# Performance work log

Hardware: AMD Instinct MI355X
Metric: run time of the kernel (lower is better)

Reference implementation:

```python
import jax, jax.numpy as jnp
import numpy as np

DIM = 1024
NUM_HEADS = 16
HEAD_DIM = DIM // NUM_HEADS
SCALE = HEAD_DIM ** (-0.5)


def setup_inputs() -> dict:
    key = jax.random.key(0)
    ks = jax.random.split(key, 10)
    b, nq, nkv = 1, 4096, 4096
    s = DIM ** -0.5
    return {
        "q": jax.random.normal(ks[0], (b, nq, DIM), jnp.float32),
        "kv": jax.random.normal(ks[1], (b, nkv, DIM), jnp.float32),
        "q_w": jax.random.normal(ks[2], (DIM, DIM), jnp.float32) * s,
        "q_b": jnp.zeros((DIM,), jnp.float32),
        "k_w": jax.random.normal(ks[3], (DIM, DIM), jnp.float32) * s,
        "k_b": jnp.zeros((DIM,), jnp.float32),
        "v_w": jax.random.normal(ks[4], (DIM, DIM), jnp.float32) * s,
        "v_b": jnp.zeros((DIM,), jnp.float32),
        "o_w": jax.random.normal(ks[5], (DIM, DIM), jnp.float32) * s,
        "o_b": jnp.zeros((DIM,), jnp.float32),
    }


def reference(q, kv, q_w, q_b, k_w, k_b, v_w, v_b, o_w, o_b):
    b, nq, _ = q.shape
    nkv = kv.shape[1]
    h, c = NUM_HEADS, HEAD_DIM
    # projections (torch Linear: x @ W^T + b); split into heads
    qh = (q @ q_w.T + q_b).reshape(b, nq, h, c).transpose(0, 2, 1, 3)   # b h nq c
    kh = (kv @ k_w.T + k_b).reshape(b, nkv, h, c).transpose(0, 2, 1, 3)  # b h nkv c
    vh = (kv @ v_w.T + v_b).reshape(b, nkv, h, c).transpose(0, 2, 1, 3)  # b h nkv c
    # full attention score matrix (non-fused, as in source)
    attn = jnp.einsum('bhqc,bhkc->bhqk', qh, kh) * SCALE
    attn = jax.nn.softmax(attn, axis=-1)
    out = jnp.einsum('bhqk,bhkc->bhqc', attn, vh)  # b h nq c
    out = out.transpose(0, 2, 1, 3).reshape(b, nq, h * c)
    out = out @ o_w.T + o_b
    return out
```

## Files before the change

### kernel.cpp

```cpp
#include <hip/hip_runtime.h>


typedef unsigned short ushort_t;
typedef unsigned short ushort4v __attribute__((ext_vector_type(4)));
typedef unsigned short ushort8 __attribute__((ext_vector_type(8)));
typedef __bf16 bf16x8 __attribute__((ext_vector_type(8)));
typedef float f32x4 __attribute__((ext_vector_type(4)));
typedef float f32x16 __attribute__((ext_vector_type(16)));
typedef unsigned int uint4v __attribute__((ext_vector_type(4)));

#define SEQ 4096
#define DIM 1024
#define NH 16
#define HD 64
#define QSCALE 0.18033688011112042f

#define LSTR 40
#define ABUF (128 * LSTR)
#define BBUF (64 * LSTR)

__device__ inline ushort_t fcvt(float f) {
    return __builtin_bit_cast(ushort_t, (__bf16)f);
}
__device__ inline bf16x8 frag_of(ushort8 t) {
    return __builtin_bit_cast(bf16x8, t);
}
__device__ inline bf16x8 lds_frag(const ushort_t* p) {
    return frag_of(*(const ushort8*)p);
}
__device__ inline unsigned pk2(float a, float b) {
    return (unsigned)fcvt(a) | ((unsigned)fcvt(b) << 16);
}
__device__ inline void plswap(unsigned& a, unsigned& b) {
    asm("v_permlane32_swap_b32 %0, %1" : "+v"(a), "+v"(b));
}
__device__ inline int swz(int row, int col) {
    return row * 64 + (col ^ ((row & 7) << 3));
}

__global__ __launch_bounds__(256) void cvt2(
    const float* __restrict__ s0, ushort_t* __restrict__ d0,
    const float* __restrict__ s1, ushort_t* __restrict__ d1, int n8)
{
    const float* s = blockIdx.y ? s1 : s0;
    ushort_t*    d = blockIdx.y ? d1 : d0;
    int i = blockIdx.x * 256 + threadIdx.x;
    if (i >= n8) return;
    const f32x4* sp = (const f32x4*)s + (size_t)i * 2;
    f32x4 a = sp[0], b = sp[1];
    ushort8 o;
    for (int k = 0; k < 4; ++k) { o[k] = fcvt(a[k]); o[k + 4] = fcvt(b[k]); }
    *((ushort8*)d + i) = o;
}

__global__ __launch_bounds__(256) void cvt4(
    const float* __restrict__ s0, ushort_t* __restrict__ d0,
    const float* __restrict__ s1, ushort_t* __restrict__ d1,
    const float* __restrict__ s2, ushort_t* __restrict__ d2,
    const float* __restrict__ s3, ushort_t* __restrict__ d3, int n8)
{
    const float* ss[4] = {s0, s1, s2, s3};
    ushort_t*    dd[4] = {d0, d1, d2, d3};
    const float* s = ss[blockIdx.y];
    ushort_t*    d = dd[blockIdx.y];
    int i = blockIdx.x * 256 + threadIdx.x;
    if (i >= n8) return;
    const f32x4* sp = (const f32x4*)s + (size_t)i * 2;
    f32x4 a = sp[0], b = sp[1];
    ushort8 o;
    for (int k = 0; k < 4; ++k) { o[k] = fcvt(a[k]); o[k + 4] = fcvt(b[k]); }
    *((ushort8*)d + i) = o;
}

__device__ __attribute__((always_inline)) inline void gemm_core(
    const ushort_t* __restrict__ A, const ushort_t* __restrict__ W,
    int m0, int n0, int tid, f32x4 (&acc)[4][2], ushort_t* sA, ushort_t* sB)
{
    const int lane = tid & 63;
    const int quad = lane >> 4;
    const int l15  = lane & 15;
    const int wm   = (tid >> 6) >> 1;
    const int wn   = (tid >> 6) & 1;

    const int ar0 = tid >> 2;
    const int ar1 = (tid + 256) >> 2;
    const int ac  = (tid & 3) << 3;
    const int br  = tid >> 2;
    const ushort_t* Ag0 = A + (size_t)(m0 + ar0) * DIM + ac;
    const ushort_t* Ag1 = A + (size_t)(m0 + ar1) * DIM + ac;
    const ushort_t* Wg  = W + (size_t)(n0 + br) * DIM + ac;
    const int la0 = ar0 * LSTR + ac, la1 = ar1 * LSTR + ac, lb = br * LSTR + ac;

    *(ushort8*)(sA + la0) = *(const ushort8*)(Ag0);
    *(ushort8*)(sA + la1) = *(const ushort8*)(Ag1);
    *(ushort8*)(sB + lb)  = *(const ushort8*)(Wg);
    __syncthreads();

    for (int it = 0; it < DIM / 32; ++it) {
        const int cur = it & 1;
        const int ktn = (it + 1) * 32;
        ushort_t* aC = sA + cur * ABUF;
        ushort_t* bC = sB + cur * BBUF;

        ushort8 ga0, ga1, gb0;
        if (ktn < DIM) {
            ga0 = *(const ushort8*)(Ag0 + ktn);
            ga1 = *(const ushort8*)(Ag1 + ktn);
            gb0 = *(const ushort8*)(Wg + ktn);
        }

        bf16x8 af[4], bf[2];
        for (int i = 0; i < 4; ++i)
            af[i] = lds_frag(aC + (wm * 64 + i * 16 + l15) * LSTR + quad * 8);
        for (int j = 0; j < 2; ++j)
            bf[j] = lds_frag(bC + (wn * 32 + j * 16 + l15) * LSTR + quad * 8);
        for (int i = 0; i < 4; ++i)
            for (int j = 0; j < 2; ++j)
                acc[i][j] = __builtin_amdgcn_mfma_f32_16x16x32_bf16(
                    af[i], bf[j], acc[i][j], 0, 0, 0);

        if (ktn < DIM) {
            ushort_t* aN = sA + (cur ^ 1) * ABUF;
            ushort_t* bN = sB + (cur ^ 1) * BBUF;
            *(ushort8*)(aN + la0) = ga0;
            *(ushort8*)(aN + la1) = ga1;
            *(ushort8*)(bN + lb)  = gb0;
        }
        __syncthreads();
    }
}

__global__ __launch_bounds__(256) void proj3(
    const ushort_t* __restrict__ Qb, const ushort_t* __restrict__ KVb,
    const ushort_t* __restrict__ qwb, const ushort_t* __restrict__ kwb,
    const ushort_t* __restrict__ vwb,
    const float* __restrict__ q_b, const float* __restrict__ k_b,
    const float* __restrict__ v_b,
    ushort_t* __restrict__ Qp, ushort_t* __restrict__ Kp,
    ushort_t* __restrict__ VpT)
{
    __shared__ __align__(16) ushort_t sA[2 * ABUF];
    __shared__ __align__(16) ushort_t sB[2 * BBUF];

    const int z = blockIdx.z;
    const ushort_t* A = z ? KVb : Qb;
    const ushort_t* W = (z == 0) ? qwb : (z == 1 ? kwb : vwb);
    const float* bias = (z == 0) ? q_b : (z == 1 ? k_b : v_b);
    const int tid = threadIdx.x;
    const int m0 = blockIdx.y * 128;
    const int n0 = blockIdx.x * 64;

    f32x4 acc[4][2] = {};
    gemm_core(A, W, m0, n0, tid, acc, sA, sB);

    const int lane = tid & 63, quad = lane >> 4, l15 = lane & 15;
    const int wm = (tid >> 6) >> 1, wn = (tid >> 6) & 1;

    if (z == 2) {
        const int TSTR = 136;
        for (int j = 0; j < 2; ++j) {
            int col = wn * 32 + j * 16 + l15;
            float bj = bias[n0 + col];
            for (int i = 0; i < 4; ++i) {
                int row = wm * 64 + i * 16 + quad * 4;
                ushort4v o4;
                for (int r = 0; r < 4; ++r) o4[r] = fcvt(acc[i][j][r] + bj);
                *(ushort4v*)(sA + col * TSTR + row) = o4;
            }
        }
        __syncthreads();
        const int vrow = tid >> 2;
        const int vc   = (tid & 3) << 3;
        ushort_t* dst = VpT + (size_t)(n0 + vrow) * SEQ + m0;
        const ushort_t* src = sA + vrow * TSTR;
        for (int k = 0; k < 4; ++k)
            *(ushort8*)(dst + vc + k * 32) = *(const ushort8*)(src + vc + k * 32);
    } else {
        const float scale = (z == 0) ? QSCALE : 1.0f;
        ushort_t* C = z ? Kp : Qp;
        for (int j = 0; j < 2; ++j) {
            int col = n0 + wn * 32 + j * 16 + l15;
            float bj = bias[col];
            for (int i = 0; i < 4; ++i) {
                int row = m0 + wm * 64 + i * 16 + quad * 4;
                for (int r = 0; r < 4; ++r)
                    C[(size_t)(row + r) * DIM + col] =
                        fcvt((acc[i][j][r] + bj) * scale);
            }
        }
    }
}

__global__ __launch_bounds__(256) void gemm_out(
    const ushort_t* __restrict__ A, const ushort_t* __restrict__ W,
    const float* __restrict__ bias, float* __restrict__ C)
{
    __shared__ __align__(16) ushort_t sA[2 * ABUF];
    __shared__ __align__(16) ushort_t sB[2 * BBUF];

    const int tid = threadIdx.x;
    const int m0 = blockIdx.y * 128;
    const int n0 = blockIdx.x * 64;

    f32x4 acc[4][2] = {};
    gemm_core(A, W, m0, n0, tid, acc, sA, sB);

    const int lane = tid & 63, quad = lane >> 4, l15 = lane & 15;
    const int wm = (tid >> 6) >> 1, wn = (tid >> 6) & 1;
    for (int j = 0; j < 2; ++j) {
        int col = n0 + wn * 32 + j * 16 + l15;
        float bj = bias[col];
        for (int i = 0; i < 4; ++i) {
            int row = m0 + wm * 64 + i * 16 + quad * 4;
            for (int r = 0; r < 4; ++r)
                C[(size_t)(row + r) * DIM + col] = acc[i][j][r] + bj;
        }
    }
}

#define TILE 4096
#define BUFE (2 * TILE)
__global__ __launch_bounds__(256, 2) void attn_kernel(
    const ushort_t* __restrict__ Q, const ushort_t* __restrict__ K,
    const ushort_t* __restrict__ VT, ushort_t* __restrict__ O)
{
    __shared__ __align__(16) ushort_t sB[2 * BUFE];

    const int tid  = threadIdx.x;
    const int w    = tid >> 6;
    const int lane = tid & 63;
    const int l31  = lane & 31;
    const int hi   = lane >> 5;
    const int h    = blockIdx.x;
    const int q0   = blockIdx.y * 128 + w * 32;
    const int hHD  = h * HD;

    const int srow0 = tid >> 3;
    const int srow1 = srow0 + 32;
    const int sch   = (tid & 7) << 3;
    const ushort_t* Kg0 = K  + (size_t)srow0 * DIM + hHD + sch;
    const ushort_t* Kg1 = K  + (size_t)srow1 * DIM + hHD + sch;
    const ushort_t* Vg0 = VT + (size_t)(hHD + srow0) * SEQ + sch;
    const ushort_t* Vg1 = VT + (size_t)(hHD + srow1) * SEQ + sch;
    const int lk0 = swz(srow0, sch), lk1 = swz(srow1, sch);

    const ushort_t* qb = Q + (size_t)(q0 + l31) * DIM + hHD + hi * 8;
    bf16x8 qf[4];
    for (int ks = 0; ks < 4; ++ks)
        qf[ks] = frag_of(*(const ushort8*)(qb + ks * 16));

    *(ushort8*)(sB + lk0)        = *(const ushort8*)(Kg0);
    *(ushort8*)(sB + lk1)        = *(const ushort8*)(Kg1);
    *(ushort8*)(sB + TILE + lk0) = *(const ushort8*)(Vg0);
    *(ushort8*)(sB + TILE + lk1) = *(const ushort8*)(Vg1);
    __syncthreads();

    f32x16 oacc[2] = {};
    float l_i = 0.f;

    for (int it = 0; it < SEQ / 64; ++it) {
        const int cur = it & 1;
        const int kvn = (it + 1) * 64;
        ushort_t* bK = sB + cur * BUFE;
        ushort_t* bV = bK + TILE;

        ushort8 gk0, gk1, gv0, gv1;
        if (kvn < SEQ) {
            gk0 = *(const ushort8*)(Kg0 + (size_t)kvn * DIM);
            gk1 = *(const ushort8*)(Kg1 + (size_t)kvn * DIM);
            gv0 = *(const ushort8*)(Vg0 + kvn);
            gv1 = *(const ushort8*)(Vg1 + kvn);
        }

        bf16x8 kf[8], vf[8];
        for (int t = 0; t < 2; ++t)
            for (int ks = 0; ks < 4; ++ks) {
                int r = t * 32 + l31;
                kf[t * 4 + ks] = lds_frag(bK + swz(r, ks * 16 + hi * 8));
            }
        for (int dt = 0; dt < 2; ++dt)
            for (int ks = 0; ks < 4; ++ks) {
                int r = dt * 32 + l31;
                vf[ks * 2 + dt] = lds_frag(bV + swz(r, ks * 16 + hi * 8));
            }

        f32x16 sacc[2] = {};
        for (int t = 0; t < 2; ++t)
            for (int ks = 0; ks < 4; ++ks)
                sacc[t] = __builtin_amdgcn_mfma_f32_32x32x16_bf16(
                    kf[t * 4 + ks], qf[ks], sacc[t], 0, 0, 0);

        float lp = 0.f;
        for (int t = 0; t < 2; ++t)
            for (int r = 0; r < 16; ++r) {
                float p = __builtin_amdgcn_exp2f(sacc[t][r]);
                sacc[t][r] = p;
                lp += p;
            }
        l_i += lp + __shfl_xor(lp, 32);

        for (int ks = 0; ks < 4; ++ks) {
            const int t = ks >> 1, s8 = (ks & 1) * 8;
            unsigned p00 = pk2(sacc[t][s8 + 0], sacc[t][s8 + 1]);
            unsigned p01 = pk2(sacc[t][s8 + 2], sacc[t][s8 + 3]);
            unsigned p10 = pk2(sacc[t][s8 + 4], sacc[t][s8 + 5]);
            unsigned p11 = pk2(sacc[t][s8 + 6], sacc[t][s8 + 7]);
            plswap(p00, p10);
            plswap(p01, p11);
            uint4v wv; wv[0] = p00; wv[1] = p01; wv[2] = p10; wv[3] = p11;
            bf16x8 pf = __builtin_bit_cast(bf16x8, wv);
            for (int dt = 0; dt < 2; ++dt)
                oacc[dt] = __builtin_amdgcn_mfma_f32_32x32x16_bf16(
                    vf[ks * 2 + dt], pf, oacc[dt], 0, 0, 0);
        }

        if (kvn < SEQ) {
            ushort_t* nB = sB + (cur ^ 1) * BUFE;
            *(ushort8*)(nB + lk0)        = gk0;
            *(ushort8*)(nB + lk1)        = gk1;
            *(ushort8*)(nB + TILE + lk0) = gv0;
            *(ushort8*)(nB + TILE + lk1) = gv1;
        }
        __syncthreads();
    }

    float inv = 1.f / l_i;
    int qrow = q0 + l31;
    for (int dt = 0; dt < 2; ++dt)
        for (int g = 0; g < 4; ++g) {
            ushort4v o4;
            for (int r = 0; r < 4; ++r) o4[r] = fcvt(oacc[dt][g * 4 + r] * inv);
            *(ushort4v*)(O + (size_t)qrow * DIM + hHD + dt * 32 + g * 8 + hi * 4) = o4;
        }
}

extern "C" void kernel_launch(void* const* d_in, const int* in_sizes, int n_in,
                              void* d_out, int out_size, void* d_ws, size_t ws_size,
                              hipStream_t stream)
{
    const float* q   = (const float*)d_in[0];
    const float* kv  = (const float*)d_in[1];
    const float* q_w = (const float*)d_in[2];
    const float* q_b = (const float*)d_in[3];
    const float* k_w = (const float*)d_in[4];
    const float* k_b = (const float*)d_in[5];
    const float* v_w = (const float*)d_in[6];
    const float* v_b = (const float*)d_in[7];
    const float* o_w = (const float*)d_in[8];
    const float* o_b = (const float*)d_in[9];
    float* out = (float*)d_out;

    const size_t SD = (size_t)SEQ * DIM;
    const size_t WW = (size_t)DIM * DIM;
    ushort_t* Qp  = (ushort_t*)d_ws;
    ushort_t* Kp  = Qp + SD;
    ushort_t* VpT = Kp + SD;
    ushort_t* AO  = VpT + SD;
    ushort_t* Qb  = AO;
    ushort_t* KVb = AO + SD;
    ushort_t* qwb = KVb + SD;
    ushort_t* kwb = qwb + WW;
    ushort_t* vwb = kwb + WW;
    ushort_t* owb = vwb + WW;

    cvt2<<<dim3((unsigned)(SD / 8 / 256), 2), 256, 0, stream>>>(
        q, Qb, kv, KVb, (int)(SD / 8));
    cvt4<<<dim3((unsigned)(WW / 8 / 256), 4), 256, 0, stream>>>(
        q_w, qwb, k_w, kwb, v_w, vwb, o_w, owb, (int)(WW / 8));

    proj3<<<dim3(DIM / 64, SEQ / 128, 3), 256, 0, stream>>>(
        Qb, KVb, qwb, kwb, vwb, q_b, k_b, v_b, Qp, Kp, VpT);
    attn_kernel<<<dim3(NH, SEQ / 128), 256, 0, stream>>>(Qp, Kp, VpT, AO);
    gemm_out<<<dim3(DIM / 64, SEQ / 128), 256, 0, stream>>>(AO, owb, o_b, out);
}
```

Before: 259.3 us.

## Rewrite projection GEMMs with direct global-to-LDS loads, swizzled tiles, larger N tile

```diff
diff --git a/kernel.cpp b/kernel.cpp
--- a/kernel.cpp
+++ b/kernel.cpp
@@ -15,10 +15,6 @@
 #define HD 64
 #define QSCALE 0.18033688011112042f
 
-#define LSTR 40
-#define ABUF (128 * LSTR)
-#define BBUF (64 * LSTR)
-
 __device__ inline ushort_t fcvt(float f) {
     return __builtin_bit_cast(ushort_t, (__bf16)f);
 }
@@ -36,6 +32,13 @@
 }
 __device__ inline int swz(int row, int col) {
     return row * 64 + (col ^ ((row & 7) << 3));
+}
+__device__ __attribute__((always_inline)) inline void gload16(
+    const ushort_t* g, ushort_t* l)
+{
+    __builtin_amdgcn_global_load_lds(
+        (const __attribute__((address_space(1))) void*)g,
+        (__attribute__((address_space(3))) void*)l, 16, 0, 0);
 }
 
 __global__ __launch_bounds__(256) void cvt2(
@@ -72,65 +75,75 @@
     *((ushort8*)d + i) = o;
 }
 
-__device__ __attribute__((always_inline)) inline void gemm_core(
+template<int BN>
+__device__ __attribute__((always_inline)) inline void gemm_core2(
     const ushort_t* __restrict__ A, const ushort_t* __restrict__ W,
-    int m0, int n0, int tid, f32x4 (&acc)[4][2], ushort_t* sA, ushort_t* sB)
-{
+    int m0, int n0, int tid, f32x4 (&acc)[4][BN / 32], ushort_t* sLDS)
+{
+    constexpr int TA = 128 * 64;
+    constexpr int TB = BN * 64;
+    ushort_t* const aB0 = sLDS;
+    ushort_t* const aB1 = sLDS + TA;
+    ushort_t* const bB0 = sLDS + 2 * TA;
+    ushort_t* const bB1 = sLDS + 2 * TA + TB;
+
+    const int w    = tid >> 6;
     const int lane = tid & 63;
     const int quad = lane >> 4;
     const int l15  = lane & 15;
-    const int wm   = (tid >> 6) >> 1;
-    const int wn   = (tid >> 6) & 1;
-
-    const int ar0 = tid >> 2;
-    const int ar1 = (tid + 256) >> 2;
-    const int ac  = (tid & 3) << 3;
-    const int br  = tid >> 2;
-    const ushort_t* Ag0 = A + (size_t)(m0 + ar0) * DIM + ac;
-    const ushort_t* Ag1 = A + (size_t)(m0 + ar1) * DIM + ac;
-    const ushort_t* Wg  = W + (size_t)(n0 + br) * DIM + ac;
-    const int la0 = ar0 * LSTR + ac, la1 = ar1 * LSTR + ac, lb = br * LSTR + ac;
-
-    *(ushort8*)(sA + la0) = *(const ushort8*)(Ag0);
-    *(ushort8*)(sA + la1) = *(const ushort8*)(Ag1);
-    *(ushort8*)(sB + lb)  = *(const ushort8*)(Wg);
+    const int wm   = w >> 1;
+    const int wn   = w & 1;
+
+    const int srow = lane >> 3;
+    const int sch  = ((lane & 7) ^ srow) << 3;
+    const ushort_t* Ag = A + (size_t)(m0 + w * 32 + srow) * DIM + sch;
+    const ushort_t* Bg = W + (size_t)(n0 + w * (BN / 4) + srow) * DIM + sch;
+    const int aOff = w * 2048;
+    const int bOff = w * (BN * 16);
+
+    for (int i = 0; i < 4; ++i)
+        gload16(Ag + (size_t)(i * 8) * DIM, aB0 + aOff + i * 512);
+    for (int i = 0; i < BN / 32; ++i)
+        gload16(Bg + (size_t)(i * 8) * DIM, bB0 + bOff + i * 512);
     __syncthreads();
 
-    for (int it = 0; it < DIM / 32; ++it) {
+    const int cxor = l15 & 7;
+    for (int it = 0; it < DIM / 64; ++it) {
         const int cur = it & 1;
-        const int ktn = (it + 1) * 32;
-        ushort_t* aC = sA + cur * ABUF;
-        ushort_t* bC = sB + cur * BBUF;
-
-        ushort8 ga0, ga1, gb0;
-        if (ktn < DIM) {
-            ga0 = *(const ushort8*)(Ag0 + ktn);
-            ga1 = *(const ushort8*)(Ag1 + ktn);
-            gb0 = *(const ushort8*)(Wg + ktn);
-        }
-
-        bf16x8 af[4], bf[2];
-        for (int i = 0; i < 4; ++i)
-            af[i] = lds_frag(aC + (wm * 64 + i * 16 + l15) * LSTR + quad * 8);
-        for (int j = 0; j < 2; ++j)
-            bf[j] = lds_frag(bC + (wn * 32 + j * 16 + l15) * LSTR + quad * 8);
-        for (int i = 0; i < 4; ++i)
-            for (int j = 0; j < 2; ++j)
-                acc[i][j] = __builtin_amdgcn_mfma_f32_16x16x32_bf16(
-                    af[i], bf[j], acc[i][j], 0, 0, 0);
-
-        if (ktn < DIM) {
-            ushort_t* aN = sA + (cur ^ 1) * ABUF;
-            ushort_t* bN = sB + (cur ^ 1) * BBUF;
-            *(ushort8*)(aN + la0) = ga0;
-            *(ushort8*)(aN + la1) = ga1;
-            *(ushort8*)(bN + lb)  = gb0;
+        ushort_t* aC = cur ? aB1 : aB0;
+        ushort_t* bC = cur ? bB1 : bB0;
+        ushort_t* aN = cur ? aB0 : aB1;
+        ushort_t* bN = cur ? bB0 : bB1;
+
+        if (it + 1 < DIM / 64) {
+            const int k0 = (it + 1) * 64;
+            for (int i = 0; i < 4; ++i)
+                gload16(Ag + k0 + (size_t)(i * 8) * DIM, aN + aOff + i * 512);
+            for (int i = 0; i < BN / 32; ++i)
+                gload16(Bg + k0 + (size_t)(i * 8) * DIM, bN + bOff + i * 512);
+        }
+
+        for (int kk = 0; kk < 2; ++kk) {
+            const int cq = kk * 4 + quad;
+            bf16x8 af[4], bf[BN / 32];
+            for (int i = 0; i < 4; ++i) {
+                int row = wm * 64 + i * 16 + l15;
+                af[i] = lds_frag(aC + row * 64 + ((cq ^ cxor) << 3));
+            }
+            for (int j = 0; j < BN / 32; ++j) {
+                int row = wn * (BN / 2) + j * 16 + l15;
+                bf[j] = lds_frag(bC + row * 64 + ((cq ^ cxor) << 3));
+            }
+            for (int i = 0; i < 4; ++i)
+                for (int j = 0; j < BN / 32; ++j)
+                    acc[i][j] = __builtin_amdgcn_mfma_f32_16x16x32_bf16(
+                        af[i], bf[j], acc[i][j], 0, 0, 0);
         }
         __syncthreads();
     }
 }
 
-__global__ __launch_bounds__(256) void proj3(
+__global__ __launch_bounds__(256, 2) void proj3(
     const ushort_t* __restrict__ Qb, const ushort_t* __restrict__ KVb,
     const ushort_t* __restrict__ qwb, const ushort_t* __restrict__ kwb,
     const ushort_t* __restrict__ vwb,
@@ -139,8 +152,7 @@
     ushort_t* __restrict__ Qp, ushort_t* __restrict__ Kp,
     ushort_t* __restrict__ VpT)
 {
-    __shared__ __align__(16) ushort_t sA[2 * ABUF];
-    __shared__ __align__(16) ushort_t sB[2 * BBUF];
+    __shared__ __align__(1024) ushort_t sLDS[32768];
 
     const int z = blockIdx.z;
     const ushort_t* A = z ? KVb : Qb;
@@ -148,38 +160,38 @@
     const float* bias = (z == 0) ? q_b : (z == 1 ? k_b : v_b);
     const int tid = threadIdx.x;
     const int m0 = blockIdx.y * 128;
-    const int n0 = blockIdx.x * 64;
-
-    f32x4 acc[4][2] = {};
-    gemm_core(A, W, m0, n0, tid, acc, sA, sB);
+    const int n0 = blockIdx.x * 128;
+
+    f32x4 acc[4][4] = {};
+    gemm_core2<128>(A, W, m0, n0, tid, acc, sLDS);
 
     const int lane = tid & 63, quad = lane >> 4, l15 = lane & 15;
     const int wm = (tid >> 6) >> 1, wn = (tid >> 6) & 1;
 
     if (z == 2) {
         const int TSTR = 136;
-        for (int j = 0; j < 2; ++j) {
-            int col = wn * 32 + j * 16 + l15;
+        for (int j = 0; j < 4; ++j) {
+            int col = wn * 64 + j * 16 + l15;
             float bj = bias[n0 + col];
             for (int i = 0; i < 4; ++i) {
                 int row = wm * 64 + i * 16 + quad * 4;
                 ushort4v o4;
                 for (int r = 0; r < 4; ++r) o4[r] = fcvt(acc[i][j][r] + bj);
-                *(ushort4v*)(sA + col * TSTR + row) = o4;
+                *(ushort4v*)(sLDS + col * TSTR + row) = o4;
             }
         }
         __syncthreads();
-        const int vrow = tid >> 2;
-        const int vc   = (tid & 3) << 3;
-        ushort_t* dst = VpT + (size_t)(n0 + vrow) * SEQ + m0;
-        const ushort_t* src = sA + vrow * TSTR;
-        for (int k = 0; k < 4; ++k)
-            *(ushort8*)(dst + vc + k * 32) = *(const ushort8*)(src + vc + k * 32);
+        const int vrow = tid >> 1;
+        const int vc   = (tid & 1) * 64;
+        ushort_t* dst = VpT + (size_t)(n0 + vrow) * SEQ + m0 + vc;
+        const ushort_t* src = sLDS + vrow * TSTR + vc;
+        for (int k = 0; k < 8; ++k)
+            *(ushort8*)(dst + k * 8) = *(const ushort8*)(src + k * 8);
     } else {
         const float scale = (z == 0) ? QSCALE : 1.0f;
         ushort_t* C = z ? Kp : Qp;
-        for (int j = 0; j < 2; ++j) {
-            int col = n0 + wn * 32 + j * 16 + l15;
+        for (int j = 0; j < 4; ++j) {
+            int col = n0 + wn * 64 + j * 16 + l15;
             float bj = bias[col];
             for (int i = 0; i < 4; ++i) {
                 int row = m0 + wm * 64 + i * 16 + quad * 4;
@@ -191,19 +203,18 @@
     }
 }
 
-__global__ __launch_bounds__(256) void gemm_out(
+__global__ __launch_bounds__(256, 2) void gemm_out(
     const ushort_t* __restrict__ A, const ushort_t* __restrict__ W,
     const float* __restrict__ bias, float* __restrict__ C)
 {
-    __shared__ __align__(16) ushort_t sA[2 * ABUF];
-    __shared__ __align__(16) ushort_t sB[2 * BBUF];
+    __shared__ __align__(1024) ushort_t sLDS[24576];
 
     const int tid = threadIdx.x;
     const int m0 = blockIdx.y * 128;
     const int n0 = blockIdx.x * 64;
 
     f32x4 acc[4][2] = {};
-    gemm_core(A, W, m0, n0, tid, acc, sA, sB);
+    gemm_core2<64>(A, W, m0, n0, tid, acc, sLDS);
 
     const int lane = tid & 63, quad = lane >> 4, l15 = lane & 15;
     const int wm = (tid >> 6) >> 1, wn = (tid >> 6) & 1;
@@ -368,7 +379,7 @@
     cvt4<<<dim3((unsigned)(WW / 8 / 256), 4), 256, 0, stream>>>(
         q_w, qwb, k_w, kwb, v_w, vwb, o_w, owb, (int)(WW / 8));
 
-    proj3<<<dim3(DIM / 64, SEQ / 128, 3), 256, 0, stream>>>(
+    proj3<<<dim3(DIM / 128, SEQ / 128, 3), 256, 0, stream>>>(
         Qb, KVb, qwb, kwb, vwb, q_b, k_b, v_b, Qp, Kp, VpT);
     attn_kernel<<<dim3(NH, SEQ / 128), 256, 0, stream>>>(Qp, Kp, VpT, AO);
     gemm_out<<<dim3(DIM / 64, SEQ / 128), 256, 0, stream>>>(AO, owb, o_b, out);
```

Result: faster. 245.3 us (-5.4%).
